# Kernel tuning notes

Hardware: AMD Instinct MI355X
Metric: run time of the kernel (lower is better)

The kernel has to match this reference:

```python
import jax, jax.numpy as jnp
import numpy as np

N_NODES = 50000
N_EDGES = 800000
IN_CH, HID_CH, OUT_CH = 100, 128, 47
ORIG_SIZE = 25000


def sage_conv(x, edge_index, w_l, b_l, w_r):
    """PyG-style SAGEConv with mean aggregation.
    out = lin_l(mean_{j in N(i)} x_j) + lin_r(x_i)
    edge_index[0]=source, edge_index[1]=target.
    """
    src, dst = edge_index[0], edge_index[1]
    n = x.shape[0]
    # gather source features, scatter-sum into targets  [N, d]
    agg = jax.ops.segment_sum(x[src], dst, num_segments=n)
    deg = jax.ops.segment_sum(jnp.ones((src.shape[0],), x.dtype), dst, num_segments=n)
    mean = agg / jnp.maximum(deg, 1.0)[:, None]
    return mean @ w_l + b_l + x @ w_r


def setup_inputs() -> dict:
    key = jax.random.key(0)
    ks = jax.random.split(key, 8)
    x = jax.random.normal(ks[0], (N_NODES, IN_CH), dtype=jnp.float32)
    edge_index = jax.random.randint(ks[1], (2, N_EDGES), 0, N_NODES, dtype=jnp.int32)
    s1 = 1.0 / np.sqrt(IN_CH)
    s2 = 1.0 / np.sqrt(HID_CH)
    w1_l = jax.random.uniform(ks[2], (IN_CH, HID_CH), jnp.float32, -s1, s1)
    b1_l = jax.random.uniform(ks[3], (HID_CH,), jnp.float32, -s1, s1)
    w1_r = jax.random.uniform(ks[4], (IN_CH, HID_CH), jnp.float32, -s1, s1)
    w2_l = jax.random.uniform(ks[5], (HID_CH, OUT_CH), jnp.float32, -s2, s2)
    b2_l = jax.random.uniform(ks[6], (OUT_CH,), jnp.float32, -s2, s2)
    w2_r = jax.random.uniform(ks[7], (HID_CH, OUT_CH), jnp.float32, -s2, s2)
    return {"x": x, "edge_index": edge_index, "original_size": ORIG_SIZE,
            "w1_l": w1_l, "b1_l": b1_l, "w1_r": w1_r,
            "w2_l": w2_l, "b2_l": b2_l, "w2_r": w2_r}


def reference(x, edge_index, original_size, w1_l, b1_l, w1_r, w2_l, b2_l, w2_r):
    h = sage_conv(x, edge_index, w1_l, b1_l, w1_r)   # [N, hidden]
    h = sage_conv(h, edge_index, w2_l, b2_l, w2_r)   # [N, out]
    logp = jax.nn.log_softmax(h, axis=1)
    return logp[:original_size]
```

## Files before the change

### kernel.cpp

```cpp
#include <hip/hip_runtime.h>
#include <hip/hip_fp16.h>
#include <math.h>

constexpr int N    = 50000;
constexpr int E    = 800000;
constexpr int CIN  = 100;
constexpr int CH   = 128;
constexpr int COUT = 47;
constexpr int NOUT = 25000;
constexpr int CP   = 48;
constexpr int NB   = (N + 255) / 256;
constexpr int TN   = 128;
constexpr int NT   = (N + TN - 1) / TN;

constexpr int AS  = 72;
constexpr int HS  = 136;
constexpr int W1K = 256;
constexpr int W2K = 128;

typedef float f32x4 __attribute__((ext_vector_type(4)));
typedef short v8s  __attribute__((ext_vector_type(8)));

__device__ __forceinline__ void bsplit(float f, ushort& h, ushort& l) {
    uint u = __float_as_uint(f);
    h = (ushort)(u >> 16);
    float fh = __uint_as_float(u & 0xffff0000u);
    l = (ushort)(__float_as_uint(f - fh) >> 16);
}

__global__ void hist_kernel(const int* __restrict__ dst, int* __restrict__ cnt,
                            int* __restrict__ rank) {
    int i = blockIdx.x * blockDim.x + threadIdx.x;
    if (i < E) rank[i] = atomicAdd(&cnt[dst[i]], 1);
}

__global__ __launch_bounds__(256) void scan_blocks(const int* __restrict__ cnt,
        int* __restrict__ row_ptr, int* __restrict__ blkSum) {
    __shared__ int s[256];
    int t = threadIdx.x;
    int i = blockIdx.x * 256 + t;
    int v = (i < N) ? cnt[i] : 0;
    s[t] = v;
    __syncthreads();
    for (int off = 1; off < 256; off <<= 1) {
        int a = s[t];
        int u = (t >= off) ? s[t - off] : 0;
        __syncthreads();
        s[t] = a + u;
        __syncthreads();
    }
    if (i < N) row_ptr[i] = s[t] - v;
    if (t == 255) blkSum[blockIdx.x] = s[255];
}

__global__ __launch_bounds__(256) void scan_apply(int* __restrict__ row_ptr,
        const int* __restrict__ blkSum) {
    __shared__ int s[256];
    int t = threadIdx.x, bid = blockIdx.x;
    int a = 0;
    for (int j = t; j < bid; j += 256) a += blkSum[j];
    s[t] = a;
    __syncthreads();
    for (int off = 128; off > 0; off >>= 1) {
        if (t < off) s[t] += s[t + off];
        __syncthreads();
    }
    int offset = s[0];
    int i = bid * 256 + t;
    if (i < N) {
        row_ptr[i] += offset;
        if (i == N - 1) row_ptr[N] = E;
    }
}

__global__ void fill_kernel(const int* __restrict__ src, const int* __restrict__ dst,
        const int* __restrict__ rank, const int* __restrict__ row_ptr,
        int* __restrict__ col) {
    int i = blockIdx.x * blockDim.x + threadIdx.x;
    if (i < E) col[row_ptr[dst[i]] + rank[i]] = src[i];
}

__global__ __launch_bounds__(256) void convert_x(const float* __restrict__ x,
        __half* __restrict__ x16) {
    int i = blockIdx.x * 256 + threadIdx.x;
    if (i < N * CIN / 4) {
        float4 v = ((const float4*)x)[i];
        __half2 h0 = __floats2half2_rn(v.x, v.y);
        __half2 h1 = __floats2half2_rn(v.z, v.w);
        union { __half2 h[2]; uint2 u; } U;
        U.h[0] = h0; U.h[1] = h1;
        ((uint2*)x16)[i] = U.u;
    }
}

__global__ __launch_bounds__(256) void prep_w(const float* __restrict__ w1l,
        const float* __restrict__ w1r, const float* __restrict__ w2l,
        const float* __restrict__ w2r, const float* __restrict__ b2l,
        ushort* __restrict__ w1T, ushort* __restrict__ w2T,
        float* __restrict__ b2cat) {
    int i = blockIdx.x * 256 + threadIdx.x;
    if (i < 128 * W1K) {
        int n = i >> 8, k = i & 255;
        float v = 0.0f;
        if (k < 100)                    v = w1l[(size_t)k * CH + n];
        else if (k >= 128 && k < 228)   v = w1r[(size_t)(k - 128) * CH + n];
        ushort h, l; bsplit(v, h, l);
        w1T[i] = h; w1T[128 * W1K + i] = l;
    } else if (i < 128 * W1K + 128 * W2K) {
        int j = i - 128 * W1K;
        int n = j >> 7, k = j & 127;
        float v = 0.0f;
        if (n < COUT)                      v = w2l[(size_t)k * COUT + n];
        else if (n >= 64 && n < 64 + COUT) v = w2r[(size_t)k * COUT + (n - 64)];
        ushort h, l; bsplit(v, h, l);
        w2T[j] = h; w2T[128 * W2K + j] = l;
    } else {
        int j = i - (128 * W1K + 128 * W2K);
        if (j < 128) b2cat[j] = (j >= 64 && j < 64 + COUT) ? b2l[j - 64] : 0.0f;
    }
}

__global__ __launch_bounds__(256) void gather1_kernel(const __half* __restrict__ x16,
        const int* __restrict__ row_ptr, const int* __restrict__ col,
        float* __restrict__ agg1) {
    int t = threadIdx.x;
    int n = blockIdx.x * 4 + (t >> 6);
    int l = t & 63, half = l >> 5, li = l & 31;
    int b = row_ptr[n], e = row_ptr[n + 1];
    float inv = 1.0f / (float)max(e - b, 1);
    const uint2* xb = (const uint2*)x16;
    bool act = li < 25;
    float4 s0 = make_float4(0.f, 0.f, 0.f, 0.f);
    float4 s1 = make_float4(0.f, 0.f, 0.f, 0.f);
    float4 s2 = make_float4(0.f, 0.f, 0.f, 0.f);
    float4 s3 = make_float4(0.f, 0.f, 0.f, 0.f);
    union { uint2 u; __half2 h[2]; } U0, U1, U2, U3;
    int j = b + half;
    for (; j + 6 < e; j += 8) {
        int c0 = col[j], c1 = col[j + 2], c2 = col[j + 4], c3 = col[j + 6];
        if (act) {
            U0.u = xb[(size_t)c0 * 25 + li];
            U1.u = xb[(size_t)c1 * 25 + li];
            U2.u = xb[(size_t)c2 * 25 + li];
            U3.u = xb[(size_t)c3 * 25 + li];
            float2 f0a = __half22float2(U0.h[0]), f0b = __half22float2(U0.h[1]);
            float2 f1a = __half22float2(U1.h[0]), f1b = __half22float2(U1.h[1]);
            float2 f2a = __half22float2(U2.h[0]), f2b = __half22float2(U2.h[1]);
            float2 f3a = __half22float2(U3.h[0]), f3b = __half22float2(U3.h[1]);
            s0.x += f0a.x; s0.y += f0a.y; s0.z += f0b.x; s0.w += f0b.y;
            s1.x += f1a.x; s1.y += f1a.y; s1.z += f1b.x; s1.w += f1b.y;
            s2.x += f2a.x; s2.y += f2a.y; s2.z += f2b.x; s2.w += f2b.y;
            s3.x += f3a.x; s3.y += f3a.y; s3.z += f3b.x; s3.w += f3b.y;
        }
    }
    for (; j < e; j += 2) {
        int c0 = col[j];
        if (act) {
            U0.u = xb[(size_t)c0 * 25 + li];
            float2 f0a = __half22float2(U0.h[0]), f0b = __half22float2(U0.h[1]);
            s0.x += f0a.x; s0.y += f0a.y; s0.z += f0b.x; s0.w += f0b.y;
        }
    }
    float4 s = make_float4(s0.x + s1.x + s2.x + s3.x,
                           s0.y + s1.y + s2.y + s3.y,
                           s0.z + s1.z + s2.z + s3.z,
                           s0.w + s1.w + s2.w + s3.w);
    s.x += __shfl_xor(s.x, 32, 64);
    s.y += __shfl_xor(s.y, 32, 64);
    s.z += __shfl_xor(s.z, 32, 64);
    s.w += __shfl_xor(s.w, 32, 64);
    if (half == 0 && act)
        ((float4*)agg1)[(size_t)n * 25 + li] = make_float4(
            s.x * inv, s.y * inv, s.z * inv, s.w * inv);
}

__global__ __launch_bounds__(256) void fused_gemm(
        const float* __restrict__ agg1, const float* __restrict__ x,
        const ushort* __restrict__ w1T, const float* __restrict__ b1l,
        const ushort* __restrict__ w2T, const float* __restrict__ b2cat,
        __half* __restrict__ gsrc16, float* __restrict__ gself) {
    __shared__ __align__(16) uint lds_u[17408];
    ushort* Ah = (ushort*)lds_u;
    ushort* Al = Ah + 128 * AS;
    ushort* Hh = (ushort*)lds_u;
    ushort* Hl = Hh + 128 * HS;

    int t = threadIdx.x;
    int lane = t & 63;
    int wv = __builtin_amdgcn_readfirstlane(t >> 6);
    int nh = wv & 1, chh = wv >> 1;
    int l15 = lane & 15, lg = lane >> 4;
    int base = blockIdx.x * TN;

    const ushort* w1Th = w1T;
    const ushort* w1Tl = w1T + 128 * W1K;
    const ushort* w2Th = w2T;
    const ushort* w2Tl = w2T + 128 * W2K;

    f32x4 acc[4][4];
    #pragma unroll
    for (int nt = 0; nt < 4; ++nt) {
        float bv = b1l[chh * 64 + nt * 16 + l15];
        #pragma unroll
        for (int mt = 0; mt < 4; ++mt)
            acc[mt][nt] = f32x4{bv, bv, bv, bv};
    }

    int srow = t >> 1, sq = t & 1;
    int nmax = N - 1 - base; if (nmax > TN - 1) nmax = TN - 1;
    int srr = srow <= nmax ? srow : nmax;

    for (int c = 0; c < 4; ++c) {
        const float* F = (c < 2) ? agg1 : x;
        const float4* Fp = (const float4*)(F + (size_t)(base + srr) * CIN);
        int cj0 = (c & 1) * 16 + sq * 8;
        #pragma unroll
        for (int q = 0; q < 8; ++q) {
            int cj = cj0 + q;
            float4 v = (cj < 25) ? Fp[cj] : make_float4(0.f, 0.f, 0.f, 0.f);
            ushort h0, h1, h2, h3, l0, l1, l2, l3;
            bsplit(v.x, h0, l0); bsplit(v.y, h1, l1);
            bsplit(v.z, h2, l2); bsplit(v.w, h3, l3);
            int di = srow * AS + sq * 32 + q * 4;
            *(uint2*)(Ah + di) = make_uint2((uint)h0 | ((uint)h1 << 16),
                                            (uint)h2 | ((uint)h3 << 16));
            *(uint2*)(Al + di) = make_uint2((uint)l0 | ((uint)l1 << 16),
                                            (uint)l2 | ((uint)l3 << 16));
        }
        __syncthreads();
        #pragma unroll
        for (int ks = 0; ks < 2; ++ks) {
            v8s ahf[4], alf[4];
            #pragma unroll
            for (int mt = 0; mt < 4; ++mt) {
                int row = nh * 64 + mt * 16 + l15;
                int ko = ks * 32 + lg * 8;
                ahf[mt] = *(const v8s*)(Ah + row * AS + ko);
                alf[mt] = *(const v8s*)(Al + row * AS + ko);
            }
            int kg = c * 64 + ks * 32 + lg * 8;
            #pragma unroll
            for (int nt = 0; nt < 4; ++nt) {
                int n = chh * 64 + nt * 16 + l15;
                v8s bhf = *(const v8s*)(w1Th + (size_t)n * W1K + kg);
                v8s blf = *(const v8s*)(w1Tl + (size_t)n * W1K + kg);
                #pragma unroll
                for (int mt = 0; mt < 4; ++mt) {
                    acc[mt][nt] = __builtin_amdgcn_mfma_f32_16x16x32_bf16(
                        ahf[mt], bhf, acc[mt][nt], 0, 0, 0);
                    acc[mt][nt] = __builtin_amdgcn_mfma_f32_16x16x32_bf16(
                        alf[mt], bhf, acc[mt][nt], 0, 0, 0);
                    acc[mt][nt] = __builtin_amdgcn_mfma_f32_16x16x32_bf16(
                        ahf[mt], blf, acc[mt][nt], 0, 0, 0);
                }
            }
        }
        __syncthreads();
    }

    #pragma unroll
    for (int mt = 0; mt < 4; ++mt) {
        #pragma unroll
        for (int nt = 0; nt < 4; ++nt) {
            int ch = chh * 64 + nt * 16 + l15;
            #pragma unroll
            for (int r = 0; r < 4; ++r) {
                int node = nh * 64 + mt * 16 + lg * 4 + r;
                ushort h, l; bsplit(acc[mt][nt][r], h, l);
                Hh[node * HS + ch] = h;
                Hl[node * HS + ch] = l;
            }
        }
    }
    __syncthreads();

    bool skip = (chh == 1) && (base >= NOUT);
    if (!skip) {
        #pragma unroll
        for (int nt = 0; nt < 4; ++nt) {
            float bv = b2cat[chh * 64 + nt * 16 + l15];
            #pragma unroll
            for (int mt = 0; mt < 4; ++mt)
                acc[mt][nt] = f32x4{bv, bv, bv, bv};
        }
        #pragma unroll
        for (int ks = 0; ks < 4; ++ks) {
            v8s ahf[4], alf[4];
            #pragma unroll
            for (int mt = 0; mt < 4; ++mt) {
                int node = nh * 64 + mt * 16 + l15;
                int ko = ks * 32 + lg * 8;
                ahf[mt] = *(const v8s*)(Hh + node * HS + ko);
                alf[mt] = *(const v8s*)(Hl + node * HS + ko);
            }
            int kg = ks * 32 + lg * 8;
            #pragma unroll
            for (int nt = 0; nt < 4; ++nt) {
                int n = chh * 64 + nt * 16 + l15;
                v8s bhf = *(const v8s*)(w2Th + (size_t)n * W2K + kg);
                v8s blf = *(const v8s*)(w2Tl + (size_t)n * W2K + kg);
                #pragma unroll
                for (int mt = 0; mt < 4; ++mt) {
                    acc[mt][nt] = __builtin_amdgcn_mfma_f32_16x16x32_bf16(
                        ahf[mt], bhf, acc[mt][nt], 0, 0, 0);
                    acc[mt][nt] = __builtin_amdgcn_mfma_f32_16x16x32_bf16(
                        alf[mt], bhf, acc[mt][nt], 0, 0, 0);
                    acc[mt][nt] = __builtin_amdgcn_mfma_f32_16x16x32_bf16(
                        ahf[mt], blf, acc[mt][nt], 0, 0, 0);
                }
            }
        }
        int lim = chh ? NOUT : N;
        #pragma unroll
        for (int nt = 0; nt < 3; ++nt) {
            int colc = nt * 16 + l15;
            #pragma unroll
            for (int mt = 0; mt < 4; ++mt) {
                #pragma unroll
                for (int r = 0; r < 4; ++r) {
                    int node = base + nh * 64 + mt * 16 + lg * 4 + r;
                    if (node < lim) {
                        if (chh) gself[(size_t)node * CP + colc] = acc[mt][nt][r];
                        else gsrc16[(size_t)node * CP + colc] =
                                 __float2half(acc[mt][nt][r]);
                    }
                }
            }
        }
    }
}

__global__ __launch_bounds__(256) void final_kernel(const __half* __restrict__ gsrc16,
        const float* __restrict__ gself, const int* __restrict__ row_ptr,
        const int* __restrict__ col, float* __restrict__ out) {
    int t = threadIdx.x;
    int n = blockIdx.x * 4 + (t >> 6);
    int c = t & 63;
    int b = row_ptr[n], e = row_ptr[n + 1];
    float inv = 1.0f / (float)max(e - b, 1);
    float a0 = 0.f, a1 = 0.f, a2 = 0.f, a3 = 0.f;
    if (c < CP) {
        int j = b;
        for (; j + 3 < e; j += 4) {
            a0 += __half2float(gsrc16[(size_t)col[j]     * CP + c]);
            a1 += __half2float(gsrc16[(size_t)col[j + 1] * CP + c]);
            a2 += __half2float(gsrc16[(size_t)col[j + 2] * CP + c]);
            a3 += __half2float(gsrc16[(size_t)col[j + 3] * CP + c]);
        }
        for (; j < e; ++j) a0 += __half2float(gsrc16[(size_t)col[j] * CP + c]);
    }
    float val = (c < COUT)
        ? (((a0 + a1) + (a2 + a3)) * inv + gself[(size_t)n * CP + c]) : -INFINITY;
    float m = val;
    #pragma unroll
    for (int off = 32; off > 0; off >>= 1) m = fmaxf(m, __shfl_xor(m, off, 64));
    float ex = (c < COUT) ? expf(val - m) : 0.f;
    float ssum = ex;
    #pragma unroll
    for (int off = 32; off > 0; off >>= 1) ssum += __shfl_xor(ssum, off, 64);
    if (c < COUT) out[(size_t)n * COUT + c] = val - m - logf(ssum);
}

extern "C" void kernel_launch(void* const* d_in, const int* in_sizes, int n_in,
                              void* d_out, int out_size, void* d_ws, size_t ws_size,
                              hipStream_t stream) {
    const float* x   = (const float*)d_in[0];
    const int*   ei  = (const int*)d_in[1];
    const int*   src = ei;
    const int*   dst = ei + E;
    const float* w1l = (const float*)d_in[3];
    const float* b1l = (const float*)d_in[4];
    const float* w1r = (const float*)d_in[5];
    const float* w2l = (const float*)d_in[6];
    const float* b2l = (const float*)d_in[7];
    const float* w2r = (const float*)d_in[8];
    float* out = (float*)d_out;

    int* cnt     = (int*)d_ws;
    int* row_ptr = cnt + N;
    int* rank    = row_ptr + N + 1;
    int* blkSum  = rank + E;
    int* col     = blkSum + NB;
    size_t intWords = (size_t)N + (N + 1) + E + NB + E;
    intWords = (intWords + 3) & ~(size_t)3;
    float* agg1   = (float*)d_ws + intWords;
    float* gself  = agg1 + (size_t)N * CIN;
    float* b2cat  = gself + (size_t)NOUT * CP;
    __half* gsrc16 = (__half*)(b2cat + 128);
    __half* x16    = gsrc16 + (size_t)N * CP;
    ushort* w1T   = (ushort*)(x16 + (size_t)N * CIN);
    ushort* w2T   = w1T + 2 * 128 * W1K;

    hipMemsetAsync(cnt, 0, (size_t)N * sizeof(int), stream);
    prep_w      <<<193, 256, 0, stream>>>(w1l, w1r, w2l, w2r, b2l, w1T, w2T, b2cat);
    convert_x   <<<(N * CIN / 4 + 255) / 256, 256, 0, stream>>>(x, x16);
    hist_kernel <<<(E + 255) / 256, 256, 0, stream>>>(dst, cnt, rank);
    scan_blocks <<<NB, 256, 0, stream>>>(cnt, row_ptr, blkSum);
    scan_apply  <<<NB, 256, 0, stream>>>(row_ptr, blkSum);
    fill_kernel <<<(E + 255) / 256, 256, 0, stream>>>(src, dst, rank, row_ptr, col);
    gather1_kernel<<<N / 4, 256, 0, stream>>>(x16, row_ptr, col, agg1);
    fused_gemm  <<<NT, 256, 0, stream>>>(agg1, x, w1T, b1l, w2T, b2cat, gsrc16, gself);
    final_kernel<<<NOUT / 4, 256, 0, stream>>>(gsrc16, gself, row_ptr, col, out);
}
```

Before: 231.6 us.

## Merge preprocessing kernels, prefetch GEMM input chunks, use nontemporal stores

Three independent preprocessing kernels (edge histogram, x fp16 conversion, weight split/transpose) are merged into one launch that dispatches on block index, which saves two launches and lets their blocks run concurrently. In the fused GEMM, the next feature chunk is loaded from global memory into registers before the current chunk is split into bf16 pairs and used, so load latency overlaps the MFMA work at the cost of more registers. Several output writes (col, agg1, gself, final out) become nontemporal stores to reduce cache pollution, though agg1 and col are read again later, so bypassing the cache may hurt those later reads.

```diff
diff --git a/kernel.cpp b/kernel.cpp
--- a/kernel.cpp
+++ b/kernel.cpp
@@ -18,6 +18,10 @@
 constexpr int W1K = 256;
 constexpr int W2K = 128;
 
+constexpr int HB = (E + 255) / 256;
+constexpr int CB = (N * CIN / 4 + 255) / 256;
+constexpr int PB = 193;
+
 typedef float f32x4 __attribute__((ext_vector_type(4)));
 typedef short v8s  __attribute__((ext_vector_type(8)));
 
@@ -28,10 +32,50 @@
     l = (ushort)(__float_as_uint(f - fh) >> 16);
 }
 
-__global__ void hist_kernel(const int* __restrict__ dst, int* __restrict__ cnt,
-                            int* __restrict__ rank) {
-    int i = blockIdx.x * blockDim.x + threadIdx.x;
-    if (i < E) rank[i] = atomicAdd(&cnt[dst[i]], 1);
+__global__ __launch_bounds__(256) void pre_kernel(
+        const int* __restrict__ dst, int* __restrict__ cnt, int* __restrict__ rank,
+        const float* __restrict__ x, __half* __restrict__ x16,
+        const float* __restrict__ w1l, const float* __restrict__ w1r,
+        const float* __restrict__ w2l, const float* __restrict__ w2r,
+        const float* __restrict__ b2l,
+        ushort* __restrict__ w1T, ushort* __restrict__ w2T,
+        float* __restrict__ b2cat) {
+    int bid = blockIdx.x, t = threadIdx.x;
+    if (bid < HB) {
+        int i = bid * 256 + t;
+        if (i < E) rank[i] = atomicAdd(&cnt[dst[i]], 1);
+    } else if (bid < HB + CB) {
+        int i = (bid - HB) * 256 + t;
+        if (i < N * CIN / 4) {
+            float4 v = ((const float4*)x)[i];
+            __half2 h0 = __floats2half2_rn(v.x, v.y);
+            __half2 h1 = __floats2half2_rn(v.z, v.w);
+            union { __half2 h[2]; uint2 u; } U;
+            U.h[0] = h0; U.h[1] = h1;
+            ((uint2*)x16)[i] = U.u;
+        }
+    } else {
+        int i = (bid - HB - CB) * 256 + t;
+        if (i < 128 * W1K) {
+            int n = i >> 8, k = i & 255;
+            float v = 0.0f;
+            if (k < 100)                    v = w1l[(size_t)k * CH + n];
+            else if (k >= 128 && k < 228)   v = w1r[(size_t)(k - 128) * CH + n];
+            ushort h, l; bsplit(v, h, l);
+            w1T[i] = h; w1T[128 * W1K + i] = l;
+        } else if (i < 128 * W1K + 128 * W2K) {
+            int j = i - 128 * W1K;
+            int n = j >> 7, k = j & 127;
+            float v = 0.0f;
+            if (n < COUT)                      v = w2l[(size_t)k * COUT + n];
+            else if (n >= 64 && n < 64 + COUT) v = w2r[(size_t)k * COUT + (n - 64)];
+            ushort h, l; bsplit(v, h, l);
+            w2T[j] = h; w2T[128 * W2K + j] = l;
+        } else {
+            int j = i - (128 * W1K + 128 * W2K);
+            if (j < 128) b2cat[j] = (j >= 64 && j < 64 + COUT) ? b2l[j - 64] : 0.0f;
+        }
+    }
 }
 
 __global__ __launch_bounds__(256) void scan_blocks(const int* __restrict__ cnt,
@@ -77,47 +121,7 @@
         const int* __restrict__ rank, const int* __restrict__ row_ptr,
         int* __restrict__ col) {
     int i = blockIdx.x * blockDim.x + threadIdx.x;
-    if (i < E) col[row_ptr[dst[i]] + rank[i]] = src[i];
-}
-
-__global__ __launch_bounds__(256) void convert_x(const float* __restrict__ x,
-        __half* __restrict__ x16) {
-    int i = blockIdx.x * 256 + threadIdx.x;
-    if (i < N * CIN / 4) {
-        float4 v = ((const float4*)x)[i];
-        __half2 h0 = __floats2half2_rn(v.x, v.y);
-        __half2 h1 = __floats2half2_rn(v.z, v.w);
-        union { __half2 h[2]; uint2 u; } U;
-        U.h[0] = h0; U.h[1] = h1;
-        ((uint2*)x16)[i] = U.u;
-    }
-}
-
-__global__ __launch_bounds__(256) void prep_w(const float* __restrict__ w1l,
-        const float* __restrict__ w1r, const float* __restrict__ w2l,
-        const float* __restrict__ w2r, const float* __restrict__ b2l,
-        ushort* __restrict__ w1T, ushort* __restrict__ w2T,
-        float* __restrict__ b2cat) {
-    int i = blockIdx.x * 256 + threadIdx.x;
-    if (i < 128 * W1K) {
-        int n = i >> 8, k = i & 255;
-        float v = 0.0f;
-        if (k < 100)                    v = w1l[(size_t)k * CH + n];
-        else if (k >= 128 && k < 228)   v = w1r[(size_t)(k - 128) * CH + n];
-        ushort h, l; bsplit(v, h, l);
-        w1T[i] = h; w1T[128 * W1K + i] = l;
-    } else if (i < 128 * W1K + 128 * W2K) {
-        int j = i - 128 * W1K;
-        int n = j >> 7, k = j & 127;
-        float v = 0.0f;
-        if (n < COUT)                      v = w2l[(size_t)k * COUT + n];
-        else if (n >= 64 && n < 64 + COUT) v = w2r[(size_t)k * COUT + (n - 64)];
-        ushort h, l; bsplit(v, h, l);
-        w2T[j] = h; w2T[128 * W2K + j] = l;
-    } else {
-        int j = i - (128 * W1K + 128 * W2K);
-        if (j < 128) b2cat[j] = (j >= 64 && j < 64 + COUT) ? b2l[j - 64] : 0.0f;
-    }
+    if (i < E) __builtin_nontemporal_store(src[i], &col[row_ptr[dst[i]] + rank[i]]);
 }
 
 __global__ __launch_bounds__(256) void gather1_kernel(const __half* __restrict__ x16,
@@ -169,9 +173,10 @@
     s.y += __shfl_xor(s.y, 32, 64);
     s.z += __shfl_xor(s.z, 32, 64);
     s.w += __shfl_xor(s.w, 32, 64);
-    if (half == 0 && act)
-        ((float4*)agg1)[(size_t)n * 25 + li] = make_float4(
-            s.x * inv, s.y * inv, s.z * inv, s.w * inv);
+    if (half == 0 && act) {
+        f32x4 r = {s.x * inv, s.y * inv, s.z * inv, s.w * inv};
+        __builtin_nontemporal_store(r, (f32x4*)agg1 + (size_t)n * 25 + li);
+    }
 }
 
 __global__ __launch_bounds__(256) void fused_gemm(
@@ -210,17 +215,34 @@
     int nmax = N - 1 - base; if (nmax > TN - 1) nmax = TN - 1;
     int srr = srow <= nmax ? srow : nmax;
 
-    for (int c = 0; c < 4; ++c) {
-        const float* F = (c < 2) ? agg1 : x;
-        const float4* Fp = (const float4*)(F + (size_t)(base + srr) * CIN);
-        int cj0 = (c & 1) * 16 + sq * 8;
+    float4 rv[8];
+    {
+        const float4* Fp = (const float4*)(agg1 + (size_t)(base + srr) * CIN);
+        int cj0 = sq * 8;
         #pragma unroll
         for (int q = 0; q < 8; ++q) {
             int cj = cj0 + q;
-            float4 v = (cj < 25) ? Fp[cj] : make_float4(0.f, 0.f, 0.f, 0.f);
+            rv[q] = (cj < 25) ? Fp[cj] : make_float4(0.f, 0.f, 0.f, 0.f);
+        }
+    }
+
+    for (int c = 0; c < 4; ++c) {
+        float4 nv[8];
+        if (c < 3) {
+            const float* F = (c + 1 < 2) ? agg1 : x;
+            const float4* Fp = (const float4*)(F + (size_t)(base + srr) * CIN);
+            int cj0 = ((c + 1) & 1) * 16 + sq * 8;
+            #pragma unroll
+            for (int q = 0; q < 8; ++q) {
+                int cj = cj0 + q;
+                nv[q] = (cj < 25) ? Fp[cj] : make_float4(0.f, 0.f, 0.f, 0.f);
+            }
+        }
+        #pragma unroll
+        for (int q = 0; q < 8; ++q) {
             ushort h0, h1, h2, h3, l0, l1, l2, l3;
-            bsplit(v.x, h0, l0); bsplit(v.y, h1, l1);
-            bsplit(v.z, h2, l2); bsplit(v.w, h3, l3);
+            bsplit(rv[q].x, h0, l0); bsplit(rv[q].y, h1, l1);
+            bsplit(rv[q].z, h2, l2); bsplit(rv[q].w, h3, l3);
             int di = srow * AS + sq * 32 + q * 4;
             *(uint2*)(Ah + di) = make_uint2((uint)h0 | ((uint)h1 << 16),
                                             (uint)h2 | ((uint)h3 << 16));
@@ -256,6 +278,10 @@
             }
         }
         __syncthreads();
+        if (c < 3) {
+            #pragma unroll
+            for (int q = 0; q < 8; ++q) rv[q] = nv[q];
+        }
     }
 
     #pragma unroll
@@ -320,7 +346,8 @@
                 for (int r = 0; r < 4; ++r) {
                     int node = base + nh * 64 + mt * 16 + lg * 4 + r;
                     if (node < lim) {
-                        if (chh) gself[(size_t)node * CP + colc] = acc[mt][nt][r];
+                        if (chh) __builtin_nontemporal_store(acc[mt][nt][r],
+                                     gself + (size_t)node * CP + colc);
                         else gsrc16[(size_t)node * CP + colc] =
                                  __float2half(acc[mt][nt][r]);
                     }
@@ -358,7 +385,9 @@
     float ssum = ex;
     #pragma unroll
     for (int off = 32; off > 0; off >>= 1) ssum += __shfl_xor(ssum, off, 64);
-    if (c < COUT) out[(size_t)n * COUT + c] = val - m - logf(ssum);
+    if (c < COUT)
+        __builtin_nontemporal_store(val - m - logf(ssum),
+                                    out + (size_t)n * COUT + c);
 }
 
 extern "C" void kernel_launch(void* const* d_in, const int* in_sizes, int n_in,
@@ -391,10 +420,10 @@
     ushort* w1T   = (ushort*)(x16 + (size_t)N * CIN);
     ushort* w2T   = w1T + 2 * 128 * W1K;
 
-    hipMemsetAsync(cnt, 0, (size_t)N * sizeof(int), stream);
-    prep_w      <<<193, 256, 0, stream>>>(w1l, w1r, w2l, w2r, b2l, w1T, w2T, b2cat);
-    convert_x   <<<(N * CIN / 4 + 255) / 256, 256, 0, stream>>>(x, x16);
-    hist_kernel <<<(E + 255) / 256, 256, 0, stream>>>(dst, cnt, rank);
+    (void)hipMemsetAsync(cnt, 0, (size_t)N * sizeof(int), stream);
+    pre_kernel  <<<HB + CB + PB, 256, 0, stream>>>(dst, cnt, rank, x, x16,
+                                                   w1l, w1r, w2l, w2r, b2l,
+                                                   w1T, w2T, b2cat);
     scan_blocks <<<NB, 256, 0, stream>>>(cnt, row_ptr, blkSum);
     scan_apply  <<<NB, 256, 0, stream>>>(row_ptr, blkSum);
     fill_kernel <<<(E + 255) / 256, 256, 0, stream>>>(src, dst, rank, row_ptr, col);
```

Result: slower. 250.2 us (+8.0%).
